# Performance work log

Hardware: AMD Instinct MI355X
Metric: run time of the kernel (lower is better)

Reference implementation:

```python
import jax, jax.numpy as jnp
import numpy as np

N = 100000
E = 1600000
F_IN = 32
HID = 16


def _sage_conv(x, src, dst, W_l, b_l, W_r):
    # PyG SAGEConv (aggr='mean', normalize=False, root_weight=True):
    #   out = lin_l(mean_{j in N(i)} x_j) + lin_r(x_i)
    # lin_l has bias, lin_r has no bias.
    n = x.shape[0]
    msg_sum = jax.ops.segment_sum(x[src], dst, num_segments=n)          # [N, d]
    deg = jax.ops.segment_sum(jnp.ones_like(dst, dtype=x.dtype), dst, num_segments=n)
    agg = msg_sum / jnp.maximum(deg, 1.0)[:, None]                      # mean, 0 for isolated nodes
    return agg @ W_l.T + b_l + x @ W_r.T


def setup_inputs() -> dict:
    key = jax.random.key(0)
    ks = jax.random.split(key, 8)
    x = jax.random.normal(ks[0], (N, F_IN), dtype=jnp.float32)
    edge_index = jax.random.randint(ks[1], (1, 2, E), 0, N, dtype=jnp.int64)
    s1 = 1.0 / np.sqrt(F_IN)
    s2 = 1.0 / np.sqrt(HID)
    W1_l = jax.random.uniform(ks[2], (HID, F_IN), jnp.float32, -s1, s1)
    b1_l = jax.random.uniform(ks[3], (HID,), jnp.float32, -s1, s1)
    W1_r = jax.random.uniform(ks[4], (HID, F_IN), jnp.float32, -s1, s1)
    W2_l = jax.random.uniform(ks[5], (F_IN, HID), jnp.float32, -s2, s2)
    b2_l = jax.random.uniform(ks[6], (F_IN,), jnp.float32, -s2, s2)
    W2_r = jax.random.uniform(ks[7], (F_IN, HID), jnp.float32, -s2, s2)
    return {"x": x, "edge_index": edge_index, "W1_l": W1_l, "b1_l": b1_l,
            "W1_r": W1_r, "W2_l": W2_l, "b2_l": b2_l, "W2_r": W2_r}


def reference(x, edge_index, W1_l, b1_l, W1_r, W2_l, b2_l, W2_r):
    ei = jnp.squeeze(edge_index, axis=0)  # [2, E]
    src, dst = ei[0], ei[1]
    h = jax.nn.relu(_sage_conv(x, src, dst, W1_l, b1_l, W1_r))
    out = _sage_conv(h, src, dst, W2_l, b2_l, W2_r)
    return out
```

## Files before the change

kernel.cpp:

```cpp
#include <hip/hip_runtime.h>

#define F_IN 32
#define HID 16
#define BSHIFT 9
#define BNODES (1 << BSHIFT)
#define CAP 10240
#define CHUNK 8192

__device__ __forceinline__ void add4(float4& a, const float4& b) {
    a.x += b.x; a.y += b.y; a.z += b.z; a.w += b.w;
}

__device__ __forceinline__ unsigned pack2(float a, float b) {
    unsigned ua = __float_as_uint(a);
    unsigned ub = __float_as_uint(b);
    ua = (ua + 0x7FFFu + ((ua >> 16) & 1u)) >> 16;
    ub = (ub + 0x7FFFu + ((ub >> 16) & 1u)) >> 16;
    return ua | (ub << 16);
}
__device__ __forceinline__ float lo2f(unsigned u) { return __uint_as_float(u << 16); }
__device__ __forceinline__ float hi2f(unsigned u) { return __uint_as_float(u & 0xFFFF0000u); }

__global__ void k_y1(const float* __restrict__ x, const float* __restrict__ W1_l,
                     unsigned* __restrict__ y1b, int N) {
    __shared__ float Ws[HID * F_IN];
    for (int i = threadIdx.x; i < HID * F_IN; i += blockDim.x) Ws[i] = W1_l[i];
    __syncthreads();
    int node = blockIdx.x * blockDim.x + threadIdx.x;
    if (node >= N) return;

    float xr[F_IN];
    const float4* xp = (const float4*)(x + (size_t)node * F_IN);
#pragma unroll
    for (int i = 0; i < F_IN / 4; i++) {
        float4 v = xp[i];
        xr[4 * i + 0] = v.x; xr[4 * i + 1] = v.y;
        xr[4 * i + 2] = v.z; xr[4 * i + 3] = v.w;
    }
    float a[HID];
#pragma unroll
    for (int o = 0; o < HID; o++) {
        float s = 0.f;
#pragma unroll
        for (int k = 0; k < F_IN; k++) s += xr[k] * Ws[o * F_IN + k];
        a[o] = s;
    }
    uint4* yp = (uint4*)(y1b + (size_t)node * 8);
    yp[0] = make_uint4(pack2(a[0], a[1]), pack2(a[2], a[3]),
                       pack2(a[4], a[5]), pack2(a[6], a[7]));
    yp[1] = make_uint4(pack2(a[8], a[9]), pack2(a[10], a[11]),
                       pack2(a[12], a[13]), pack2(a[14], a[15]));
}

__global__ void k_part(const int* __restrict__ ei, int* __restrict__ bucketCursor,
                       unsigned* __restrict__ bucketBuf, int E) {
    __shared__ int cnt[256];
    __shared__ int runBase[256];
    __shared__ int cur[256];
    int tid = threadIdx.x;
    int e0 = blockIdx.x * CHUNK;
    int e1 = min(e0 + CHUNK, E);

    cnt[tid] = 0;
    __syncthreads();
    for (int e = e0 + tid; e < e1; e += 256) {
        int d = ei[E + e];
        atomicAdd(&cnt[d >> BSHIFT], 1);
    }
    __syncthreads();
    int c = cnt[tid];
    runBase[tid] = c ? atomicAdd(&bucketCursor[tid], c) : 0;
    cur[tid] = 0;
    __syncthreads();
    for (int e = e0 + tid; e < e1; e += 256) {
        int d = ei[E + e];
        int s = ei[e];
        int b = d >> BSHIFT;
        int pos = runBase[b] + atomicAdd(&cur[b], 1);
        if (pos < CAP)
            bucketBuf[(size_t)b * CAP + pos] =
                ((unsigned)(d & (BNODES - 1)) << 17) | (unsigned)s;
    }
}

__global__ void __launch_bounds__(256) k_csr(const int* __restrict__ bucketCursor,
                                             unsigned* __restrict__ bucketBuf,
                                             int* __restrict__ rs, int* __restrict__ deg,
                                             int N) {
    __shared__ unsigned stage[CAP];
    __shared__ int hist[BNODES];
    __shared__ int scan[BNODES];
    __shared__ int cur[BNODES];
    int b = blockIdx.x;
    int tid = threadIdx.x;
    int nE = min(bucketCursor[b], CAP);
    unsigned* buf = bucketBuf + (size_t)b * CAP;

    for (int i = tid; i < nE; i += 256) stage[i] = buf[i];
    hist[tid] = 0; hist[tid + 256] = 0;
    __syncthreads();
    for (int i = tid; i < nE; i += 256) atomicAdd(&hist[stage[i] >> 17], 1);
    __syncthreads();

    int i0 = tid, i1 = tid + 256;
    scan[i0] = hist[i0]; scan[i1] = hist[i1];
    __syncthreads();
    for (int off = 1; off < BNODES; off <<= 1) {
        int v0 = (i0 >= off) ? scan[i0 - off] : 0;
        int v1 = (i1 >= off) ? scan[i1 - off] : 0;
        __syncthreads();
        scan[i0] += v0; scan[i1] += v1;
        __syncthreads();
    }
    int ex0 = scan[i0] - hist[i0];
    int ex1 = scan[i1] - hist[i1];
    cur[i0] = ex0; cur[i1] = ex1;
    int n0 = (b << BSHIFT) + i0;
    int n1 = (b << BSHIFT) + i1;
    if (n0 < N) { rs[n0] = b * CAP + ex0; deg[n0] = hist[i0]; }
    if (n1 < N) { rs[n1] = b * CAP + ex1; deg[n1] = hist[i1]; }
    __syncthreads();

    for (int i = tid; i < nE; i += 256) {
        unsigned r = stage[i];
        int pos = atomicAdd(&cur[r >> 17], 1);
        buf[pos] = r & 0x1FFFFu;
    }
}

#define WS1 33
__global__ void k_agg1(const unsigned* __restrict__ y1b, const float* __restrict__ x,
                       const unsigned* __restrict__ col, const int* __restrict__ rs,
                       const int* __restrict__ deg, const float* __restrict__ W1_r,
                       const float* __restrict__ b1, unsigned* __restrict__ hb, int N) {
    __shared__ float Ws[HID * WS1];
    __shared__ float bs[HID];
    for (int i = threadIdx.x; i < HID * F_IN; i += blockDim.x)
        Ws[(i >> 5) * WS1 + (i & 31)] = W1_r[i];
    if (threadIdx.x < HID) bs[threadIdx.x] = b1[threadIdx.x];
    __syncthreads();
    int gid = blockIdx.x * blockDim.x + threadIdx.x;
    int node = gid >> 2;
    int c = gid & 3;
    if (node >= N) return;

    int start = rs[node];
    int dg = deg[node];
    const uint2* yv = (const uint2*)y1b;
    float4 a0 = make_float4(0,0,0,0), a1 = a0, a2 = a0, a3 = a0;
    int j = 0;
    for (; j + 8 <= dg; j += 8) {
        unsigned s0 = col[start + j + 0];
        unsigned s1 = col[start + j + 1];
        unsigned s2 = col[start + j + 2];
        unsigned s3 = col[start + j + 3];
        unsigned s4 = col[start + j + 4];
        unsigned s5 = col[start + j + 5];
        unsigned s6 = col[start + j + 6];
        unsigned s7 = col[start + j + 7];
        uint2 v0 = yv[(size_t)s0 * 4 + c];
        uint2 v1 = yv[(size_t)s1 * 4 + c];
        uint2 v2 = yv[(size_t)s2 * 4 + c];
        uint2 v3 = yv[(size_t)s3 * 4 + c];
        uint2 v4 = yv[(size_t)s4 * 4 + c];
        uint2 v5 = yv[(size_t)s5 * 4 + c];
        uint2 v6 = yv[(size_t)s6 * 4 + c];
        uint2 v7 = yv[(size_t)s7 * 4 + c];
        add4(a0, make_float4(lo2f(v0.x), hi2f(v0.x), lo2f(v0.y), hi2f(v0.y)));
        add4(a1, make_float4(lo2f(v1.x), hi2f(v1.x), lo2f(v1.y), hi2f(v1.y)));
        add4(a2, make_float4(lo2f(v2.x), hi2f(v2.x), lo2f(v2.y), hi2f(v2.y)));
        add4(a3, make_float4(lo2f(v3.x), hi2f(v3.x), lo2f(v3.y), hi2f(v3.y)));
        add4(a0, make_float4(lo2f(v4.x), hi2f(v4.x), lo2f(v4.y), hi2f(v4.y)));
        add4(a1, make_float4(lo2f(v5.x), hi2f(v5.x), lo2f(v5.y), hi2f(v5.y)));
        add4(a2, make_float4(lo2f(v6.x), hi2f(v6.x), lo2f(v6.y), hi2f(v6.y)));
        add4(a3, make_float4(lo2f(v7.x), hi2f(v7.x), lo2f(v7.y), hi2f(v7.y)));
    }
    for (; j < dg; j++) {
        unsigned s = col[start + j];
        uint2 v = yv[(size_t)s * 4 + c];
        add4(a0, make_float4(lo2f(v.x), hi2f(v.x), lo2f(v.y), hi2f(v.y)));
    }
    add4(a0, a1); add4(a2, a3); add4(a0, a2);
    float inv = 1.0f / (float)(dg > 0 ? dg : 1);
    float m[4] = {a0.x * inv, a0.y * inv, a0.z * inv, a0.w * inv};

    float xr[F_IN];
    const float4* xp = (const float4*)(x + (size_t)node * F_IN);
#pragma unroll
    for (int i = 0; i < F_IN / 4; i++) {
        float4 v = xp[i];
        xr[4 * i + 0] = v.x; xr[4 * i + 1] = v.y;
        xr[4 * i + 2] = v.z; xr[4 * i + 3] = v.w;
    }
    float a[4];
#pragma unroll
    for (int jj = 0; jj < 4; jj++) {
        int o = c * 4 + jj;
        float s = m[jj] + bs[o];
#pragma unroll
        for (int k = 0; k < F_IN; k++) s += xr[k] * Ws[o * WS1 + k];
        a[jj] = fmaxf(s, 0.0f);
    }
    ((uint2*)hb)[(size_t)node * 4 + c] = make_uint2(pack2(a[0], a[1]), pack2(a[2], a[3]));
}

#define WS2 17
__global__ void k_l2(const unsigned* __restrict__ hb, const unsigned* __restrict__ col,
                     const int* __restrict__ rs, const int* __restrict__ deg,
                     const float* __restrict__ W2_l, const float* __restrict__ b2,
                     const float* __restrict__ W2_r, float* __restrict__ out, int N) {
    __shared__ float Wl[F_IN * WS2];
    __shared__ float Wr[F_IN * WS2];
    __shared__ float bs[F_IN];
    __shared__ float mld[64][HID + 1];
    for (int i = threadIdx.x; i < F_IN * HID; i += blockDim.x) {
        int r = i >> 4, q = i & 15;
        Wl[r * WS2 + q] = W2_l[i];
        Wr[r * WS2 + q] = W2_r[i];
    }
    if (threadIdx.x < F_IN) bs[threadIdx.x] = b2[threadIdx.x];
    __syncthreads();

    int tid = threadIdx.x;
    int ln = tid >> 2;
    int c = tid & 3;
    int node = blockIdx.x * 64 + ln;

    if (node < N) {
        int start = rs[node];
        int dg = deg[node];
        const uint2* hv = (const uint2*)hb;
        float4 a0 = make_float4(0,0,0,0), a1 = a0, a2 = a0, a3 = a0;
        int j = 0;
        for (; j + 8 <= dg; j += 8) {
            unsigned s0 = col[start + j + 0];
            unsigned s1 = col[start + j + 1];
            unsigned s2 = col[start + j + 2];
            unsigned s3 = col[start + j + 3];
            unsigned s4 = col[start + j + 4];
            unsigned s5 = col[start + j + 5];
            unsigned s6 = col[start + j + 6];
            unsigned s7 = col[start + j + 7];
            uint2 v0 = hv[(size_t)s0 * 4 + c];
            uint2 v1 = hv[(size_t)s1 * 4 + c];
            uint2 v2 = hv[(size_t)s2 * 4 + c];
            uint2 v3 = hv[(size_t)s3 * 4 + c];
            uint2 v4 = hv[(size_t)s4 * 4 + c];
            uint2 v5 = hv[(size_t)s5 * 4 + c];
            uint2 v6 = hv[(size_t)s6 * 4 + c];
            uint2 v7 = hv[(size_t)s7 * 4 + c];
            add4(a0, make_float4(lo2f(v0.x), hi2f(v0.x), lo2f(v0.y), hi2f(v0.y)));
            add4(a1, make_float4(lo2f(v1.x), hi2f(v1.x), lo2f(v1.y), hi2f(v1.y)));
            add4(a2, make_float4(lo2f(v2.x), hi2f(v2.x), lo2f(v2.y), hi2f(v2.y)));
            add4(a3, make_float4(lo2f(v3.x), hi2f(v3.x), lo2f(v3.y), hi2f(v3.y)));
            add4(a0, make_float4(lo2f(v4.x), hi2f(v4.x), lo2f(v4.y), hi2f(v4.y)));
            add4(a1, make_float4(lo2f(v5.x), hi2f(v5.x), lo2f(v5.y), hi2f(v5.y)));
            add4(a2, make_float4(lo2f(v6.x), hi2f(v6.x), lo2f(v6.y), hi2f(v6.y)));
            add4(a3, make_float4(lo2f(v7.x), hi2f(v7.x), lo2f(v7.y), hi2f(v7.y)));
        }
        for (; j < dg; j++) {
            unsigned s = col[start + j];
            uint2 v = hv[(size_t)s * 4 + c];
            add4(a0, make_float4(lo2f(v.x), hi2f(v.x), lo2f(v.y), hi2f(v.y)));
        }
        add4(a0, a1); add4(a2, a3); add4(a0, a2);
        float inv = 1.0f / (float)(dg > 0 ? dg : 1);
        mld[ln][c * 4 + 0] = a0.x * inv;
        mld[ln][c * 4 + 1] = a0.y * inv;
        mld[ln][c * 4 + 2] = a0.z * inv;
        mld[ln][c * 4 + 3] = a0.w * inv;
    }
    __syncthreads();
    if (node >= N) return;

    float hr[HID];
    const uint4* hp = (const uint4*)(hb + (size_t)node * 8);
    uint4 u0 = hp[0], u1 = hp[1];
    hr[0] = lo2f(u0.x); hr[1] = hi2f(u0.x); hr[2] = lo2f(u0.y); hr[3] = hi2f(u0.y);
    hr[4] = lo2f(u0.z); hr[5] = hi2f(u0.z); hr[6] = lo2f(u0.w); hr[7] = hi2f(u0.w);
    hr[8] = lo2f(u1.x); hr[9] = hi2f(u1.x); hr[10] = lo2f(u1.y); hr[11] = hi2f(u1.y);
    hr[12] = lo2f(u1.z); hr[13] = hi2f(u1.z); hr[14] = lo2f(u1.w); hr[15] = hi2f(u1.w);

    float m[HID];
#pragma unroll
    for (int k = 0; k < HID; k++) m[k] = mld[ln][k];

    int og = c * 8;
    float a[8];
#pragma unroll
    for (int jj = 0; jj < 8; jj++) {
        int o = og + jj;
        float s = bs[o];
#pragma unroll
        for (int k = 0; k < HID; k++)
            s += m[k] * Wl[o * WS2 + k] + hr[k] * Wr[o * WS2 + k];
        a[jj] = s;
    }
    float4* op = (float4*)(out + (size_t)node * F_IN + og);
    op[0] = make_float4(a[0], a[1], a[2], a[3]);
    op[1] = make_float4(a[4], a[5], a[6], a[7]);
}

extern "C" void kernel_launch(void* const* d_in, const int* in_sizes, int n_in,
                              void* d_out, int out_size, void* d_ws, size_t ws_size,
                              hipStream_t stream) {
    const float* x    = (const float*)d_in[0];
    const int*   ei   = (const int*)d_in[1];
    const float* W1_l = (const float*)d_in[2];
    const float* b1   = (const float*)d_in[3];
    const float* W1_r = (const float*)d_in[4];
    const float* W2_l = (const float*)d_in[5];
    const float* b2   = (const float*)d_in[6];
    const float* W2_r = (const float*)d_in[7];
    float* out = (float*)d_out;

    const int N = in_sizes[0] / F_IN;
    const int E = in_sizes[1] / 2;
    const int nbuckets = (N + BNODES - 1) >> BSHIFT;

    int* bucketCursor = (int*)d_ws;
    int* rs   = bucketCursor + 256;
    int* deg  = rs + N;
    unsigned* bucketBuf = (unsigned*)(deg + N);
    unsigned* y1b = bucketBuf + (size_t)nbuckets * CAP;
    unsigned* hb  = y1b + (size_t)N * 8;

    hipMemsetAsync(bucketCursor, 0, 256 * sizeof(int), stream);

    const int B = 256;
    const int nodeBlocks = (N + B - 1) / B;
    const int partBlocks = (E + CHUNK - 1) / CHUNK;
    const int aggBlocks = (4 * N + B - 1) / B;
    const int l2Blocks = (N + 63) / 64;

    k_y1<<<nodeBlocks, B, 0, stream>>>(x, W1_l, y1b, N);
    k_part<<<partBlocks, B, 0, stream>>>(ei, bucketCursor, bucketBuf, E);
    k_csr<<<nbuckets, B, 0, stream>>>(bucketCursor, bucketBuf, rs, deg, N);
    k_agg1<<<aggBlocks, B, 0, stream>>>(y1b, x, bucketBuf, rs, deg, W1_r, b1, hb, N);
    k_l2<<<l2Blocks, B, 0, stream>>>(hb, bucketBuf, rs, deg, W2_l, b2, W2_r, out, N);
}
```

Baseline: 181.2 us.

## Split neighbor lists across two thread groups per node and stage dst indices in LDS

Both aggregation kernels now give each node 8 threads instead of 4, splitting its neighbor list into two halves whose partial sums are combined with a lane shuffle. This doubles memory-level parallelism for the gathers, which matters because average degree is around 16. The layer-2 output stage is remapped so all 8 threads each compute 4 outputs. The partition kernel caches dst indices in shared memory so the second pass does not reread them from global memory. The cost is more threads and blocks per node and idle half-groups during the dense epilogue of layer 1.

New measurement: 182.2 us. Within noise of the previous version (+0.6%).

```diff
diff --git a/kernel.cpp b/kernel.cpp
--- a/kernel.cpp
+++ b/kernel.cpp
@@ -52,11 +52,13 @@
                        pack2(a[12], a[13]), pack2(a[14], a[15]));
 }
 
-__global__ void k_part(const int* __restrict__ ei, int* __restrict__ bucketCursor,
-                       unsigned* __restrict__ bucketBuf, int E) {
+__global__ void __launch_bounds__(256) k_part(const int* __restrict__ ei,
+                                              int* __restrict__ bucketCursor,
+                                              unsigned* __restrict__ bucketBuf, int E) {
     __shared__ int cnt[256];
     __shared__ int runBase[256];
     __shared__ int cur[256];
+    __shared__ unsigned dstStage[CHUNK];
     int tid = threadIdx.x;
     int e0 = blockIdx.x * CHUNK;
     int e1 = min(e0 + CHUNK, E);
@@ -64,7 +66,8 @@
     cnt[tid] = 0;
     __syncthreads();
     for (int e = e0 + tid; e < e1; e += 256) {
-        int d = ei[E + e];
+        unsigned d = (unsigned)ei[E + e];
+        dstStage[e - e0] = d;
         atomicAdd(&cnt[d >> BSHIFT], 1);
     }
     __syncthreads();
@@ -73,13 +76,12 @@
     cur[tid] = 0;
     __syncthreads();
     for (int e = e0 + tid; e < e1; e += 256) {
-        int d = ei[E + e];
-        int s = ei[e];
+        unsigned d = dstStage[e - e0];
+        unsigned s = (unsigned)ei[e];
         int b = d >> BSHIFT;
         int pos = runBase[b] + atomicAdd(&cur[b], 1);
         if (pos < CAP)
-            bucketBuf[(size_t)b * CAP + pos] =
-                ((unsigned)(d & (BNODES - 1)) << 17) | (unsigned)s;
+            bucketBuf[(size_t)b * CAP + pos] = ((d & (BNODES - 1u)) << 17) | s;
     }
 }
 
@@ -129,10 +131,14 @@
 }
 
 #define WS1 33
-__global__ void k_agg1(const unsigned* __restrict__ y1b, const float* __restrict__ x,
-                       const unsigned* __restrict__ col, const int* __restrict__ rs,
-                       const int* __restrict__ deg, const float* __restrict__ W1_r,
-                       const float* __restrict__ b1, unsigned* __restrict__ hb, int N) {
+__global__ void __launch_bounds__(256) k_agg1(const unsigned* __restrict__ y1b,
+                                              const float* __restrict__ x,
+                                              const unsigned* __restrict__ col,
+                                              const int* __restrict__ rs,
+                                              const int* __restrict__ deg,
+                                              const float* __restrict__ W1_r,
+                                              const float* __restrict__ b1,
+                                              unsigned* __restrict__ hb, int N) {
     __shared__ float Ws[HID * WS1];
     __shared__ float bs[HID];
     for (int i = threadIdx.x; i < HID * F_IN; i += blockDim.x)
@@ -140,16 +146,21 @@
     if (threadIdx.x < HID) bs[threadIdx.x] = b1[threadIdx.x];
     __syncthreads();
     int gid = blockIdx.x * blockDim.x + threadIdx.x;
-    int node = gid >> 2;
-    int c = gid & 3;
+    int node = gid >> 3;
+    int c = threadIdx.x & 3;
+    int e = (threadIdx.x >> 2) & 1;
     if (node >= N) return;
 
     int start = rs[node];
     int dg = deg[node];
+    int half = (dg + 1) >> 1;
+    int jb = e ? half : 0;
+    int je = e ? dg : half;
+
     const uint2* yv = (const uint2*)y1b;
     float4 a0 = make_float4(0,0,0,0), a1 = a0, a2 = a0, a3 = a0;
-    int j = 0;
-    for (; j + 8 <= dg; j += 8) {
+    int j = jb;
+    for (; j + 8 <= je; j += 8) {
         unsigned s0 = col[start + j + 0];
         unsigned s1 = col[start + j + 1];
         unsigned s2 = col[start + j + 2];
@@ -175,12 +186,18 @@
         add4(a2, make_float4(lo2f(v6.x), hi2f(v6.x), lo2f(v6.y), hi2f(v6.y)));
         add4(a3, make_float4(lo2f(v7.x), hi2f(v7.x), lo2f(v7.y), hi2f(v7.y)));
     }
-    for (; j < dg; j++) {
+    for (; j < je; j++) {
         unsigned s = col[start + j];
         uint2 v = yv[(size_t)s * 4 + c];
         add4(a0, make_float4(lo2f(v.x), hi2f(v.x), lo2f(v.y), hi2f(v.y)));
     }
     add4(a0, a1); add4(a2, a3); add4(a0, a2);
+    a0.x += __shfl_xor(a0.x, 4);
+    a0.y += __shfl_xor(a0.y, 4);
+    a0.z += __shfl_xor(a0.z, 4);
+    a0.w += __shfl_xor(a0.w, 4);
+    if (e) return;
+
     float inv = 1.0f / (float)(dg > 0 ? dg : 1);
     float m[4] = {a0.x * inv, a0.y * inv, a0.z * inv, a0.w * inv};
 
@@ -205,14 +222,18 @@
 }
 
 #define WS2 17
-__global__ void k_l2(const unsigned* __restrict__ hb, const unsigned* __restrict__ col,
-                     const int* __restrict__ rs, const int* __restrict__ deg,
-                     const float* __restrict__ W2_l, const float* __restrict__ b2,
-                     const float* __restrict__ W2_r, float* __restrict__ out, int N) {
+__global__ void __launch_bounds__(256) k_l2(const unsigned* __restrict__ hb,
+                                            const unsigned* __restrict__ col,
+                                            const int* __restrict__ rs,
+                                            const int* __restrict__ deg,
+                                            const float* __restrict__ W2_l,
+                                            const float* __restrict__ b2,
+                                            const float* __restrict__ W2_r,
+                                            float* __restrict__ out, int N) {
     __shared__ float Wl[F_IN * WS2];
     __shared__ float Wr[F_IN * WS2];
     __shared__ float bs[F_IN];
-    __shared__ float mld[64][HID + 1];
+    __shared__ float mld[32][HID + 1];
     for (int i = threadIdx.x; i < F_IN * HID; i += blockDim.x) {
         int r = i >> 4, q = i & 15;
         Wl[r * WS2 + q] = W2_l[i];
@@ -222,17 +243,21 @@
     __syncthreads();
 
     int tid = threadIdx.x;
-    int ln = tid >> 2;
+    int ln = tid >> 3;
     int c = tid & 3;
-    int node = blockIdx.x * 64 + ln;
+    int e = (tid >> 2) & 1;
+    int node = blockIdx.x * 32 + ln;
 
     if (node < N) {
         int start = rs[node];
         int dg = deg[node];
+        int half = (dg + 1) >> 1;
+        int jb = e ? half : 0;
+        int je = e ? dg : half;
         const uint2* hv = (const uint2*)hb;
         float4 a0 = make_float4(0,0,0,0), a1 = a0, a2 = a0, a3 = a0;
-        int j = 0;
-        for (; j + 8 <= dg; j += 8) {
+        int j = jb;
+        for (; j + 8 <= je; j += 8) {
             unsigned s0 = col[start + j + 0];
             unsigned s1 = col[start + j + 1];
             unsigned s2 = col[start + j + 2];
@@ -258,23 +283,32 @@
             add4(a2, make_float4(lo2f(v6.x), hi2f(v6.x), lo2f(v6.y), hi2f(v6.y)));
             add4(a3, make_float4(lo2f(v7.x), hi2f(v7.x), lo2f(v7.y), hi2f(v7.y)));
         }
-        for (; j < dg; j++) {
+        for (; j < je; j++) {
             unsigned s = col[start + j];
             uint2 v = hv[(size_t)s * 4 + c];
             add4(a0, make_float4(lo2f(v.x), hi2f(v.x), lo2f(v.y), hi2f(v.y)));
         }
         add4(a0, a1); add4(a2, a3); add4(a0, a2);
-        float inv = 1.0f / (float)(dg > 0 ? dg : 1);
-        mld[ln][c * 4 + 0] = a0.x * inv;
-        mld[ln][c * 4 + 1] = a0.y * inv;
-        mld[ln][c * 4 + 2] = a0.z * inv;
-        mld[ln][c * 4 + 3] = a0.w * inv;
-    }
-    __syncthreads();
-    if (node >= N) return;
+        a0.x += __shfl_xor(a0.x, 4);
+        a0.y += __shfl_xor(a0.y, 4);
+        a0.z += __shfl_xor(a0.z, 4);
+        a0.w += __shfl_xor(a0.w, 4);
+        if (!e) {
+            float inv = 1.0f / (float)(dg > 0 ? dg : 1);
+            mld[ln][c * 4 + 0] = a0.x * inv;
+            mld[ln][c * 4 + 1] = a0.y * inv;
+            mld[ln][c * 4 + 2] = a0.z * inv;
+            mld[ln][c * 4 + 3] = a0.w * inv;
+        }
+    }
+    __syncthreads();
+
+    int node2 = blockIdx.x * 32 + (tid >> 3);
+    if (node2 >= N) return;
+    int oc = tid & 7;
 
     float hr[HID];
-    const uint4* hp = (const uint4*)(hb + (size_t)node * 8);
+    const uint4* hp = (const uint4*)(hb + (size_t)node2 * 8);
     uint4 u0 = hp[0], u1 = hp[1];
     hr[0] = lo2f(u0.x); hr[1] = hi2f(u0.x); hr[2] = lo2f(u0.y); hr[3] = hi2f(u0.y);
     hr[4] = lo2f(u0.z); hr[5] = hi2f(u0.z); hr[6] = lo2f(u0.w); hr[7] = hi2f(u0.w);
@@ -283,22 +317,19 @@
 
     float m[HID];
 #pragma unroll
-    for (int k = 0; k < HID; k++) m[k] = mld[ln][k];
-
-    int og = c * 8;
-    float a[8];
-#pragma unroll
-    for (int jj = 0; jj < 8; jj++) {
-        int o = og + jj;
+    for (int k = 0; k < HID; k++) m[k] = mld[tid >> 3][k];
+
+    float a[4];
+#pragma unroll
+    for (int jj = 0; jj < 4; jj++) {
+        int o = oc * 4 + jj;
         float s = bs[o];
 #pragma unroll
         for (int k = 0; k < HID; k++)
             s += m[k] * Wl[o * WS2 + k] + hr[k] * Wr[o * WS2 + k];
         a[jj] = s;
     }
-    float4* op = (float4*)(out + (size_t)node * F_IN + og);
-    op[0] = make_float4(a[0], a[1], a[2], a[3]);
-    op[1] = make_float4(a[4], a[5], a[6], a[7]);
+    ((float4*)out)[(size_t)node2 * (F_IN / 4) + oc] = make_float4(a[0], a[1], a[2], a[3]);
 }
 
 extern "C" void kernel_launch(void* const* d_in, const int* in_sizes, int n_in,
@@ -330,8 +361,8 @@
     const int B = 256;
     const int nodeBlocks = (N + B - 1) / B;
     const int partBlocks = (E + CHUNK - 1) / CHUNK;
-    const int aggBlocks = (4 * N + B - 1) / B;
-    const int l2Blocks = (N + 63) / 64;
+    const int aggBlocks = (8 * N + B - 1) / B;
+    const int l2Blocks = (N + 31) / 32;
 
     k_y1<<<nodeBlocks, B, 0, stream>>>(x, W1_l, y1b, N);
     k_part<<<partBlocks, B, 0, stream>>>(ei, bucketCursor, bucketBuf, E);
```
